# Optimization experiments

Measured on AMD Instinct MI355X. Metric: run time of the kernel, lower is better.

## Reference

```python
import jax, jax.numpy as jnp
import numpy as np

HEADS = 8
DIM_HEADS = 64
M_DIM = 512
X_DIM = 512
MEM_NUM = 512
N = 16384
PERCENT = 0.25
LAY_NUMBER = 2       # outer refinement iterations
CROSS_LAYERS = 2     # layers inside M_cross_layers
EPS = 1e-5


def setup_inputs() -> dict:
    key = jax.random.key(0)
    ks = jax.random.split(key, 8)
    data = jax.random.normal(ks[0], (N, X_DIM), dtype=jnp.float32)
    Memory = jax.random.normal(ks[1], (MEM_NUM, M_DIM), dtype=jnp.float32)
    # to_kv: Linear(X_dim, 2*kv_dim, bias=False); kv_dim = heads*dim_heads
    Wkv = jax.random.normal(ks[2], (X_DIM, 2 * HEADS * DIM_HEADS), dtype=jnp.float32) * 0.02
    # per cross layer: to_q (no bias) and mutl_heads (with bias)
    Wq = jax.random.normal(ks[3], (CROSS_LAYERS, M_DIM, HEADS * DIM_HEADS), dtype=jnp.float32) * 0.02
    Wm = jax.random.normal(ks[4], (CROSS_LAYERS, HEADS * DIM_HEADS, M_DIM), dtype=jnp.float32) * 0.02
    bm = jnp.zeros((CROSS_LAYERS, M_DIM), dtype=jnp.float32)
    return {"data": data, "Memory": Memory, "Wkv": Wkv, "Wq": Wq, "Wm": Wm, "bm": bm, "istest": 0}


def _layer_norm(x):
    # F.layer_norm over last dim, no affine params
    mu = jnp.mean(x, axis=-1, keepdims=True)
    var = jnp.var(x, axis=-1, keepdims=True)
    return (x - mu) * jax.lax.rsqrt(var + EPS)


def _cross_layer(M, X, Wkv, Wq_l, Wm_l, bm_l):
    # cross_att + residual + layernorm (SublayerConnection); FFN is dead code in source
    q = (M @ Wq_l).reshape(MEM_NUM, HEADS, DIM_HEADS).transpose(1, 0, 2)      # [h, m, dh]
    kv = X @ Wkv                                                              # [n, 2*h*dh]
    k, v = jnp.split(kv, 2, axis=-1)
    k = k.reshape(-1, HEADS, DIM_HEADS).transpose(1, 0, 2)                    # [h, n, dh]
    v = v.reshape(-1, HEADS, DIM_HEADS).transpose(1, 0, 2)
    sim = jnp.einsum('hid,hjd->hij', q, k) * (DIM_HEADS ** -0.5)              # [h, m, n]
    att = jax.nn.softmax(sim, axis=-1)
    o = jnp.einsum('hij,hjd->hid', att, v)                                    # [h, m, dh]
    o = o.transpose(1, 0, 2).reshape(MEM_NUM, HEADS * DIM_HEADS)
    out = o @ Wm_l + bm_l                                                     # [m, M_dim]
    return _layer_norm(out + M)


def _cross_layers(M, X, Wkv, Wq, Wm, bm):
    for l in range(CROSS_LAYERS):
        M = _cross_layer(M, X, Wkv, Wq[l], Wm[l], bm[l])
    return M


def _calucate_sim(data, M):
    # per-sample landmark similarity: max scaled dot product against memory rows
    logits = (data @ M.T) * (DIM_HEADS ** -0.5)   # [N, mem]
    return jnp.max(logits, axis=-1)               # [N]


def _calucate_emb(data, M):
    logits = (data @ M.T) * (DIM_HEADS ** -0.5)   # [N, mem]
    logp = jax.nn.log_softmax(logits, axis=-1)
    p = jnp.exp(logp)
    out_ebs = p @ M                               # soft memory readout [N, M_dim]
    result_loss = -jnp.mean(jnp.max(logp, axis=-1))
    lse = jax.scipy.special.logsumexp(logits, axis=-1)
    zloss = jnp.mean(lse ** 2)                    # router-style z-loss
    return out_ebs, result_loss, zloss


def _select(data, sim_M, k):
    _, top_idx = jax.lax.top_k(sim_M, k)
    X = jnp.zeros_like(data)
    return X.at[top_idx].set(data[top_idx])


def reference(data, Memory, Wkv, Wq, Wm, bm, istest):
    M = Memory
    sim_M = _calucate_sim(data, M)
    percent_count = int(data.shape[0] * PERCENT)
    if not istest:
        X = _select(data, sim_M, percent_count)
        for _ in range(LAY_NUMBER):
            M = _cross_layers(M, X, Wkv, Wq, Wm, bm)
            sim_M = _calucate_sim(data, M)
            X = _select(data, sim_M, percent_count)
    out_ebs, result_loss, zloss = _calucate_emb(data, M)
    return (sim_M, out_ebs, result_loss, zloss)
```

## Files before the change

### kernel.cpp

```cpp
#include <hip/hip_runtime.h>
#include <cstdint>

#define N_DATA 16384
#define DIM 512
#define MEM 512
#define KSEL 4096
#define NH 8
#define DH 64
#define KVDIM 1024
#define SCALE 0.125f
#define ZCNT 12288.0f
#define LN_EPS 1e-5f
#define NSPLIT 4

typedef unsigned short u16;
using short8 = __attribute__((ext_vector_type(8))) short;
using f32x4  = __attribute__((ext_vector_type(4))) float;

__device__ __forceinline__ unsigned fenc(float x) {
    unsigned u = __float_as_uint(x);
    return (u & 0x80000000u) ? ~u : (u | 0x80000000u);
}
__device__ __forceinline__ u16 f2bf(float x) {
    unsigned u = __float_as_uint(x);
    u += 0x7fffu + ((u >> 16) & 1u);
    return (u16)(u >> 16);
}
__device__ __forceinline__ float bf2f(u16 h) { return __uint_as_float(((unsigned)h) << 16); }

__device__ __forceinline__ float waveSum(float v) {
#pragma unroll
    for (int o = 32; o > 0; o >>= 1) v += __shfl_down(v, o, 64);
    return v;
}
__device__ float blockSum(float v) {
    __shared__ float sh[4];
    __syncthreads();
    v = waveSum(v);
    if ((threadIdx.x & 63) == 0) sh[threadIdx.x >> 6] = v;
    __syncthreads();
    if (threadIdx.x == 0) { float s = sh[0]; for (int i = 1; i < 4; ++i) s += sh[i]; sh[0] = s; }
    __syncthreads();
    return sh[0];
}

template<int ROWS, int NW, bool GATHER>
__device__ __forceinline__ void stage_tile(const u16* __restrict__ src, int ld, int k0,
                                           int row0, const int* __restrict__ gidx,
                                           u16* lds, int wave)
{
    constexpr int NI = ROWS / 16;
    const int lane = threadIdx.x & 63;
#pragma unroll
    for (int i = wave; i < NI; i += NW) {
        const int ch = i * 64 + lane;
        const int r = ch >> 2, cc = ch & 3;
        int rg = row0 + r;
        if (GATHER) rg = gidx[rg];
        const u16* g = src + (long)rg * ld + k0 + cc * 8;
        u16* l = lds + i * 512;
        __builtin_amdgcn_global_load_lds((const __attribute__((address_space(1))) void*)g,
                                         (__attribute__((address_space(3))) void*)l,
                                         16, 0, 0);
    }
}

template<int WM, int WN, bool GATHER, int EPI, bool BIAS>
__global__ __launch_bounds__(WM * WN * 64)
void mfma_gemm(const u16* __restrict__ A, const u16* __restrict__ B,
               const float* __restrict__ bias, const int* __restrict__ gidx,
               void* __restrict__ Cv, unsigned* __restrict__ simenc,
               int K, int lda, int ldb, int ldc,
               long zsA, long zsB, long zsC, int zdiv, long zsplitC, float alpha)
{
    constexpr int BM = WM * 64, BN = WN * 64, NW = WM * WN;
    __shared__ __align__(16) u16 As[BM * 32];
    __shared__ __align__(16) u16 Bs[BN * 32];

    const int t = threadIdx.x;
    const int wave = t >> 6, lane = t & 63;
    const int wr = wave / WN, wc = wave % WN;
    const int l15 = lane & 15, l4 = lane >> 4;
    const int bm0 = blockIdx.x * BM, bn0 = blockIdx.y * BN;
    const int zs = (int)blockIdx.z % zdiv;
    const int zh = (int)blockIdx.z / zdiv;
    A += (long)zh * zsA;
    B += (long)zh * zsB;

    f32x4 acc[4][4];
#pragma unroll
    for (int i = 0; i < 4; ++i)
#pragma unroll
        for (int j = 0; j < 4; ++j)
#pragma unroll
            for (int r = 0; r < 4; ++r) acc[i][j][r] = 0.f;

    const int Kd = K / zdiv;
    const int kbeg = zs * Kd;
    for (int k0 = kbeg; k0 < kbeg + Kd; k0 += 32) {
        stage_tile<BM, NW, GATHER>(A, lda, k0, bm0, gidx, As, wave);
        stage_tile<BN, NW, false>(B, ldb, k0, bn0, nullptr, Bs, wave);
        __syncthreads();
        short8 a[4], b[4];
#pragma unroll
        for (int fm = 0; fm < 4; ++fm)
            a[fm] = *(const short8*)(As + (wr * 64 + fm * 16 + l15) * 32 + l4 * 8);
#pragma unroll
        for (int fn = 0; fn < 4; ++fn)
            b[fn] = *(const short8*)(Bs + (wc * 64 + fn * 16 + l15) * 32 + l4 * 8);
#pragma unroll
        for (int fm = 0; fm < 4; ++fm)
#pragma unroll
            for (int fn = 0; fn < 4; ++fn)
                acc[fm][fn] = __builtin_amdgcn_mfma_f32_16x16x32_bf16(a[fm], b[fn], acc[fm][fn], 0, 0, 0);
        __syncthreads();
    }

    if (EPI == 2) {
#pragma unroll
        for (int fm = 0; fm < 4; ++fm)
#pragma unroll
            for (int r = 0; r < 4; ++r) {
                float mx = acc[fm][0][r];
#pragma unroll
                for (int fn = 1; fn < 4; ++fn) mx = fmaxf(mx, acc[fm][fn][r]);
#pragma unroll
                for (int o = 8; o >= 1; o >>= 1) mx = fmaxf(mx, __shfl_xor(mx, o, 64));
                if (l15 == 0) {
                    const int row = bm0 + wr * 64 + fm * 16 + l4 * 4 + r;
                    atomicMax(simenc + row, fenc(alpha * mx));
                }
            }
    } else if (EPI == 0) {
        float* C = (float*)Cv + (long)zh * zsC + (long)zs * zsplitC;
#pragma unroll
        for (int fm = 0; fm < 4; ++fm)
#pragma unroll
            for (int fn = 0; fn < 4; ++fn)
#pragma unroll
                for (int r = 0; r < 4; ++r) {
                    const int row = bm0 + wr * 64 + fm * 16 + l4 * 4 + r;
                    const int col = bn0 + wc * 64 + fn * 16 + l15;
                    float v = alpha * acc[fm][fn][r];
                    if (BIAS) v += bias[col];
                    C[(long)row * ldc + col] = v;
                }
    } else {
        u16* C = (u16*)Cv + (long)zh * zsC + (long)zs * zsplitC;
#pragma unroll
        for (int fm = 0; fm < 4; ++fm)
#pragma unroll
            for (int fn = 0; fn < 4; ++fn)
#pragma unroll
                for (int r = 0; r < 4; ++r) {
                    const int row = bm0 + wr * 64 + fm * 16 + l4 * 4 + r;
                    const int col = bn0 + wc * 64 + fn * 16 + l15;
                    float v = alpha * acc[fm][fn][r];
                    if (BIAS) v += bias[col];
                    C[(long)row * ldc + col] = f2bf(v);
                }
    }
}

__global__ __launch_bounds__(512)
void mfma_gemm_sm(const u16* __restrict__ A, const u16* __restrict__ B,
                  u16* __restrict__ Obf, float* __restrict__ simf,
                  float* __restrict__ lse, float* __restrict__ mlp, float alpha)
{
    __shared__ __align__(16) u16 As[64 * 32];
    __shared__ __align__(16) u16 Bs[512 * 32];
    const int t = threadIdx.x, wave = t >> 6, lane = t & 63;
    const int wc = wave;
    const int l15 = lane & 15, l4 = lane >> 4;
    const int bm0 = blockIdx.x * 64;

    f32x4 acc[4][4];
#pragma unroll
    for (int i = 0; i < 4; ++i)
#pragma unroll
        for (int j = 0; j < 4; ++j)
#pragma unroll
            for (int r = 0; r < 4; ++r) acc[i][j][r] = 0.f;

    for (int k0 = 0; k0 < 512; k0 += 32) {
        stage_tile<64, 8, false>(A, 512, k0, bm0, nullptr, As, wave);
        stage_tile<512, 8, false>(B, 512, k0, 0, nullptr, Bs, wave);
        __syncthreads();
        short8 a[4], b[4];
#pragma unroll
        for (int fm = 0; fm < 4; ++fm)
            a[fm] = *(const short8*)(As + (fm * 16 + l15) * 32 + l4 * 8);
#pragma unroll
        for (int fn = 0; fn < 4; ++fn)
            b[fn] = *(const short8*)(Bs + (wc * 64 + fn * 16 + l15) * 32 + l4 * 8);
#pragma unroll
        for (int fm = 0; fm < 4; ++fm)
#pragma unroll
            for (int fn = 0; fn < 4; ++fn)
                acc[fm][fn] = __builtin_amdgcn_mfma_f32_16x16x32_bf16(a[fm], b[fn], acc[fm][fn], 0, 0, 0);
        __syncthreads();
    }

    float* red  = (float*)As;
    float* rowv = (float*)Bs;

#pragma unroll
    for (int fm = 0; fm < 4; ++fm)
#pragma unroll
        for (int r = 0; r < 4; ++r) {
            float mx = alpha * acc[fm][0][r];
#pragma unroll
            for (int fn = 1; fn < 4; ++fn) mx = fmaxf(mx, alpha * acc[fm][fn][r]);
#pragma unroll
            for (int o = 1; o <= 8; o <<= 1) mx = fmaxf(mx, __shfl_xor(mx, o, 64));
            if (l15 == 0) red[(fm * 16 + l4 * 4 + r) * 8 + wc] = mx;
        }
    __syncthreads();
    if (t < 64) {
        float mx = red[t * 8];
#pragma unroll
        for (int j = 1; j < 8; ++j) mx = fmaxf(mx, red[t * 8 + j]);
        rowv[t] = mx;
    }
    __syncthreads();
#pragma unroll
    for (int fm = 0; fm < 4; ++fm)
#pragma unroll
        for (int r = 0; r < 4; ++r) {
            const int rl = fm * 16 + l4 * 4 + r;
            const float m = rowv[rl];
            float s = 0.f;
#pragma unroll
            for (int fn = 0; fn < 4; ++fn) s += __expf(alpha * acc[fm][fn][r] - m);
#pragma unroll
            for (int o = 1; o <= 8; o <<= 1) s += __shfl_xor(s, o, 64);
            if (l15 == 0) red[rl * 8 + wc] = s;
        }
    __syncthreads();
    if (t < 64) {
        float s = 0.f;
#pragma unroll
        for (int j = 0; j < 8; ++j) s += red[t * 8 + j];
        const float m = rowv[t];
        const float l = m + __logf(s);
        const int gr = bm0 + t;
        simf[gr] = m; lse[gr] = l; mlp[gr] = m - l;
        rowv[64 + t] = l;
    }
    __syncthreads();
#pragma unroll
    for (int fm = 0; fm < 4; ++fm)
#pragma unroll
        for (int r = 0; r < 4; ++r) {
            const int rl = fm * 16 + l4 * 4 + r;
            const float l = rowv[64 + rl];
#pragma unroll
            for (int fn = 0; fn < 4; ++fn) {
                const int col = wc * 64 + fn * 16 + l15;
                Obf[(long)(bm0 + rl) * 512 + col] = f2bf(__expf(alpha * acc[fm][fn][r] - l));
            }
        }
}

__global__ __launch_bounds__(256)
void flash_att(const u16* __restrict__ Mbf, const u16* __restrict__ WqT,
               const u16* __restrict__ KV, const u16* __restrict__ VT,
               float* __restrict__ oPart, float* __restrict__ mPart,
               float* __restrict__ lPart)
{
    __shared__ __align__(16) u16 Qs[64 * 64];
    __shared__ __align__(16) u16 Ks[2][64 * 64];
    __shared__ __align__(16) u16 Vs[2][64 * 64];
    __shared__ __align__(16) u16 Ps[4][16 * 72];

    const int qt = blockIdx.x, h = blockIdx.y, sp = blockIdx.z;
    const int t = threadIdx.x, wave = t >> 6, lane = t & 63;
    const int l15 = lane & 15, l4 = lane >> 4;

    const u16* Kg = KV + ((long)sp * 1024) * 1024 + h * 64;
    const u16* Vg = VT + ((long)h * 64) * 4096 + sp * 1024;

    auto stageKV = [&](int kt, int buf) {
        const u16* Kt = Kg + (long)(kt * 64) * 1024;
        const u16* Vt = Vg + kt * 64;
#pragma unroll
        for (int i = wave; i < 8; i += 4) {
            const int ch = i * 64 + lane, r = ch >> 3, s = ch & 7;
            __builtin_amdgcn_global_load_lds(
                (const __attribute__((address_space(1))) void*)(Kt + (long)r * 1024 + ((s ^ (r & 7)) * 8)),
                (__attribute__((address_space(3))) void*)(Ks[buf] + i * 512), 16, 0, 0);
        }
#pragma unroll
        for (int i = wave; i < 8; i += 4) {
            const int ch = i * 64 + lane, r = ch >> 3, s = ch & 7;
            __builtin_amdgcn_global_load_lds(
                (const __attribute__((address_space(1))) void*)(Vt + (long)r * 4096 + ((s ^ (r & 7)) * 8)),
                (__attribute__((address_space(3))) void*)(Vs[buf] + i * 512), 16, 0, 0);
        }
    };

    stageKV(0, 0);

    f32x4 accq[4];
#pragma unroll
    for (int fn = 0; fn < 4; ++fn)
#pragma unroll
        for (int r = 0; r < 4; ++r) accq[fn][r] = 0.f;
    {
        const u16* Ag = Mbf + (long)(qt * 64 + wave * 16 + l15) * 512 + l4 * 8;
        const u16* Bg = WqT + (long)(h * 64 + l15) * 512 + l4 * 8;
#pragma unroll 4
        for (int k0 = 0; k0 < 512; k0 += 32) {
            const short8 a = *(const short8*)(Ag + k0);
#pragma unroll
            for (int fn = 0; fn < 4; ++fn) {
                const short8 b = *(const short8*)(Bg + (long)fn * 16 * 512 + k0);
                accq[fn] = __builtin_amdgcn_mfma_f32_16x16x32_bf16(a, b, accq[fn], 0, 0, 0);
            }
        }
    }
#pragma unroll
    for (int fn = 0; fn < 4; ++fn)
#pragma unroll
        for (int r = 0; r < 4; ++r) {
            const int qrow = wave * 16 + l4 * 4 + r;
            const int col = fn * 16 + l15;
            Qs[qrow * 64 + (((col >> 3) ^ (qrow & 7)) << 3) + (col & 7)] = f2bf(accq[fn][r]);
        }
    __syncthreads();

    const int qr = wave * 16 + l15;
    short8 qf0 = *(const short8*)(Qs + qr * 64 + ((0 * 4 + l4) ^ (qr & 7)) * 8);
    short8 qf1 = *(const short8*)(Qs + qr * 64 + ((1 * 4 + l4) ^ (qr & 7)) * 8);

    float m = -3.0e38f, lsum = 0.f;
    f32x4 acc_o[4];
#pragma unroll
    for (int nf = 0; nf < 4; ++nf)
#pragma unroll
        for (int r = 0; r < 4; ++r) acc_o[nf][r] = 0.f;

    u16* myP = &Ps[wave][0];
    constexpr int NT = KSEL / 64 / NSPLIT;
    int cur = 0;

    for (int kt = 0; kt < NT; ++kt) {
        if (kt + 1 < NT) stageKV(kt + 1, cur ^ 1);
        const u16* Kc = Ks[cur];
        const u16* Vc = Vs[cur];
        f32x4 acc_s[4];
#pragma unroll
        for (int mf = 0; mf < 4; ++mf) {
#pragma unroll
            for (int r = 0; r < 4; ++r) acc_s[mf][r] = 0.f;
            const int kr = mf * 16 + l15;
            const short8 ka0 = *(const short8*)(Kc + kr * 64 + ((0 * 4 + l4) ^ (kr & 7)) * 8);
            const short8 ka1 = *(const short8*)(Kc + kr * 64 + ((1 * 4 + l4) ^ (kr & 7)) * 8);
            acc_s[mf] = __builtin_amdgcn_mfma_f32_16x16x32_bf16(ka0, qf0, acc_s[mf], 0, 0, 0);
            acc_s[mf] = __builtin_amdgcn_mfma_f32_16x16x32_bf16(ka1, qf1, acc_s[mf], 0, 0, 0);
        }
        float sv[16];
#pragma unroll
        for (int mf = 0; mf < 4; ++mf)
#pragma unroll
            for (int r = 0; r < 4; ++r) sv[mf * 4 + r] = SCALE * acc_s[mf][r];
        float pm = sv[0];
#pragma unroll
        for (int j = 1; j < 16; ++j) pm = fmaxf(pm, sv[j]);
        pm = fmaxf(pm, __shfl_xor(pm, 16, 64));
        pm = fmaxf(pm, __shfl_xor(pm, 32, 64));
        const float mnew = fmaxf(m, pm);
        const float corr = __expf(m - mnew);
        float rs = 0.f;
#pragma unroll
        for (int j = 0; j < 16; ++j) { sv[j] = __expf(sv[j] - mnew); rs += sv[j]; }
        rs += __shfl_xor(rs, 16, 64);
        rs += __shfl_xor(rs, 32, 64);
        lsum = lsum * corr + rs;
        m = mnew;
        const float cf0 = __shfl(corr, l4 * 4 + 0, 64);
        const float cf1 = __shfl(corr, l4 * 4 + 1, 64);
        const float cf2 = __shfl(corr, l4 * 4 + 2, 64);
        const float cf3 = __shfl(corr, l4 * 4 + 3, 64);
#pragma unroll
        for (int nf = 0; nf < 4; ++nf) {
            acc_o[nf][0] *= cf0; acc_o[nf][1] *= cf1;
            acc_o[nf][2] *= cf2; acc_o[nf][3] *= cf3;
        }
#pragma unroll
        for (int mf = 0; mf < 4; ++mf) {
            ushort4 pw;
            pw.x = f2bf(sv[mf * 4 + 0]); pw.y = f2bf(sv[mf * 4 + 1]);
            pw.z = f2bf(sv[mf * 4 + 2]); pw.w = f2bf(sv[mf * 4 + 3]);
            *(ushort4*)(myP + l15 * 72 + mf * 16 + l4 * 4) = pw;
        }
#pragma unroll
        for (int ks = 0; ks < 2; ++ks) {
            const short8 pa = *(const short8*)(myP + l15 * 72 + ks * 32 + l4 * 8);
#pragma unroll
            for (int nf = 0; nf < 4; ++nf) {
                const int dr = nf * 16 + l15;
                const short8 vb = *(const short8*)(Vc + dr * 64 + ((ks * 4 + l4) ^ (dr & 7)) * 8);
                acc_o[nf] = __builtin_amdgcn_mfma_f32_16x16x32_bf16(pa, vb, acc_o[nf], 0, 0, 0);
            }
        }
        __syncthreads();
        cur ^= 1;
    }

    float* ob = oPart + (((long)sp * NH + h) * 8 + qt) * 4096;
#pragma unroll
    for (int nf = 0; nf < 4; ++nf)
#pragma unroll
        for (int r = 0; r < 4; ++r)
            ob[(wave * 16 + l4 * 4 + r) * 64 + nf * 16 + l15] = acc_o[nf][r];
    if (lane < 16) {
        const int qi = wave * 16 + lane;
        mPart[((sp * NH + h) * 8 + qt) * 64 + qi] = m;
        lPart[((sp * NH + h) * 8 + qt) * 64 + qi] = lsum;
    }
}

__global__ __launch_bounds__(256)
void flash_combine(const float* __restrict__ oPart, const float* __restrict__ mPart,
                   const float* __restrict__ lPart, u16* __restrict__ o_bf)
{
    const int qt = blockIdx.x & 7, h = blockIdx.x >> 3;
    const int t = threadIdx.x;
    const int q = t >> 2, d0 = (t & 3) << 4;
    float mi[NSPLIT], li[NSPLIT];
#pragma unroll
    for (int sp = 0; sp < NSPLIT; ++sp) {
        const int sb = ((sp * NH + h) * 8 + qt) * 64 + q;
        mi[sp] = mPart[sb];
        li[sp] = lPart[sb];
    }
    float ms = 0.f;
#pragma unroll
    for (int sp = 0; sp < NSPLIT; ++sp) ms = fmaxf(ms, mi[sp]);
    float denom = ZCNT * __expf(-ms);
    float f[NSPLIT];
#pragma unroll
    for (int sp = 0; sp < NSPLIT; ++sp) { f[sp] = __expf(mi[sp] - ms); denom += li[sp] * f[sp]; }
    const float inv = 1.f / denom;
    float o[16];
#pragma unroll
    for (int j = 0; j < 16; ++j) o[j] = 0.f;
#pragma unroll
    for (int sp = 0; sp < NSPLIT; ++sp) {
        const float* ob = oPart + (((long)sp * NH + h) * 8 + qt) * 4096 + q * 64 + d0;
        const float fs = f[sp] * inv;
#pragma unroll
        for (int j = 0; j < 16; j += 4) {
            const float4 v = *(const float4*)(ob + j);
            o[j] += fs * v.x; o[j + 1] += fs * v.y; o[j + 2] += fs * v.z; o[j + 3] += fs * v.w;
        }
    }
    u16* op = o_bf + (qt * 64 + q) * 512 + h * 64 + d0;
#pragma unroll
    for (int j = 0; j < 16; j += 4) {
        ushort4 w4;
        w4.x = f2bf(o[j]); w4.y = f2bf(o[j + 1]); w4.z = f2bf(o[j + 2]); w4.w = f2bf(o[j + 3]);
        *(ushort4*)(op + j) = w4;
    }
}

__global__ __launch_bounds__(256)
void conv_f32_bf(const float* __restrict__ s, u16* __restrict__ d, int n)
{
    const int i = (blockIdx.x * 256 + threadIdx.x) * 4;
    if (i >= n) return;
    const float4 v = *(const float4*)(s + i);
    ushort4 o;
    o.x = f2bf(v.x); o.y = f2bf(v.y); o.z = f2bf(v.z); o.w = f2bf(v.w);
    *(ushort4*)(d + i) = o;
}

template<bool INBF>
__global__ __launch_bounds__(256)
void transpose_bf(const void* __restrict__ Sv, u16* __restrict__ D,
                  int Rr, int Cc, int ldS)
{
    __shared__ float tile[32][33];
    const int c0 = blockIdx.x * 32, r0 = blockIdx.y * 32;
    const int tx = threadIdx.x & 31, ty = threadIdx.x >> 5;
#pragma unroll
    for (int j = 0; j < 32; j += 8) {
        const int r = r0 + ty + j, c = c0 + tx;
        float v = INBF ? bf2f(((const u16*)Sv)[(long)r * ldS + c])
                       : ((const float*)Sv)[(long)r * ldS + c];
        tile[ty + j][tx] = v;
    }
    __syncthreads();
#pragma unroll
    for (int j = 0; j < 32; j += 8) {
        const int cO = c0 + ty + j, rO = r0 + tx;
        D[(long)cO * Rr + rO] = f2bf(tile[tx][ty + j]);
    }
}

__global__ __launch_bounds__(256)
void transpose_w4(const float* __restrict__ Wq, const float* __restrict__ Wm,
                  u16* __restrict__ WqT, u16* __restrict__ WmT)
{
    const int z = blockIdx.z;
    const float* S = (z < 2) ? (Wq + (long)z * DIM * DIM) : (Wm + (long)(z - 2) * DIM * DIM);
    u16* D = (z < 2) ? (WqT + (long)z * DIM * DIM) : (WmT + (long)(z - 2) * DIM * DIM);
    __shared__ float tile[32][33];
    const int c0 = blockIdx.x * 32, r0 = blockIdx.y * 32;
    const int tx = threadIdx.x & 31, ty = threadIdx.x >> 5;
#pragma unroll
    for (int j = 0; j < 32; j += 8)
        tile[ty + j][tx] = S[(long)(r0 + ty + j) * DIM + c0 + tx];
    __syncthreads();
#pragma unroll
    for (int j = 0; j < 32; j += 8)
        D[(long)(c0 + ty + j) * DIM + r0 + tx] = f2bf(tile[tx][ty + j]);
}

__device__ __forceinline__ unsigned scan1024_excl(unsigned v, unsigned* wsum)
{
    const int lane = threadIdx.x & 63, wv = threadIdx.x >> 6;
    __syncthreads();
    unsigned x = v;
#pragma unroll
    for (int o = 1; o < 64; o <<= 1) {
        unsigned y = __shfl_up(x, o, 64);
        if (lane >= o) x += y;
    }
    if (lane == 63) wsum[wv] = x;
    __syncthreads();
    if (threadIdx.x < 16) {
        unsigned w2 = wsum[threadIdx.x];
#pragma unroll
        for (int o = 1; o < 16; o <<= 1) {
            unsigned y = __shfl_up(w2, o, 64);
            if ((int)threadIdx.x >= o) w2 += y;
        }
        wsum[threadIdx.x] = w2;
    }
    __syncthreads();
    const unsigned off = (wv > 0) ? wsum[wv - 1] : 0u;
    return off + x - v;
}

#define SEL_T 1024
#define SEL_CH (N_DATA / SEL_T)
__global__ __launch_bounds__(SEL_T)
void select_topk(const unsigned* __restrict__ key, int* __restrict__ idxo, int k)
{
    __shared__ unsigned whist[16][256];
    __shared__ unsigned hist[256];
    __shared__ unsigned wsum[16];
    __shared__ unsigned sh_bin, sh_r;
    const int t = threadIdx.x;
    const int wv = t >> 6;
    const int base = t * SEL_CH;

    unsigned kreg[SEL_CH];
#pragma unroll
    for (int c = 0; c < SEL_CH; ++c) kreg[c] = key[base + c];

    unsigned prefix = 0, mask = 0;
    unsigned r = (unsigned)k;
    for (int p = 3; p >= 0; --p) {
        __syncthreads();
        for (int i = t; i < 16 * 256; i += SEL_T) ((unsigned*)whist)[i] = 0u;
        __syncthreads();
#pragma unroll
        for (int c = 0; c < SEL_CH; ++c) {
            const unsigned kv = kreg[c];
            if ((kv & mask) == prefix)
                atomicAdd(&whist[wv][(kv >> (p * 8)) & 255u], 1u);
        }
        __syncthreads();
        if (t < 256) {
            unsigned s = 0;
#pragma unroll
            for (int wq = 0; wq < 16; ++wq) s += whist[wq][t];
            hist[t] = s;
        }
        __syncthreads();
        if (t < 64) {
            const int b0 = 255 - 4 * t;
            const unsigned c = hist[b0] + hist[b0 - 1] + hist[b0 - 2] + hist[b0 - 3];
            unsigned x = c;
#pragma unroll
            for (int o = 1; o < 64; o <<= 1) {
                unsigned y = __shfl_up(x, o, 64);
                if (t >= o) x += y;
            }
            const unsigned pre = x - c;
            if (pre < r && r <= x) {
                unsigned cum = pre;
#pragma unroll
                for (int j = 0; j < 4; ++j) {
                    const int b = b0 - j;
                    cum += hist[b];
                    if (cum >= r) { sh_bin = (unsigned)b; sh_r = r - (cum - hist[b]); break; }
                }
            }
        }
        __syncthreads();
        prefix |= sh_bin << (p * 8);
        mask |= 255u << (p * 8);
        r = sh_r;
    }
    const unsigned thr = prefix;
    const unsigned ties = r;

    unsigned ceq = 0;
#pragma unroll
    for (int c = 0; c < SEL_CH; ++c) ceq += (kreg[c] == thr) ? 1u : 0u;
    const unsigned eqbase = scan1024_excl(ceq, wsum);
    unsigned eq = eqbase, csel = 0;
#pragma unroll
    for (int c = 0; c < SEL_CH; ++c) {
        const unsigned kv = kreg[c];
        bool s;
        if (kv == thr) { s = (eq < ties); ++eq; }
        else s = (kv > thr);
        csel += s ? 1u : 0u;
    }
    unsigned pos = scan1024_excl(csel, wsum);
    eq = eqbase;
#pragma unroll
    for (int c = 0; c < SEL_CH; ++c) {
        const unsigned kv = kreg[c];
        bool s;
        if (kv == thr) { s = (eq < ties); ++eq; }
        else s = (kv > thr);
        if (s) idxo[pos++] = base + c;
    }
}

__global__ __launch_bounds__(256)
void ln_add_k(const float* __restrict__ outp, const float* __restrict__ Min,
              float* __restrict__ Mout, u16* __restrict__ Mbf)
{
    const int r = blockIdx.x;
    const int t = threadIdx.x;
    float x0 = outp[r * DIM + t] + Min[r * DIM + t];
    float x1 = outp[r * DIM + t + 256] + Min[r * DIM + t + 256];
    float s = blockSum(x0 + x1);
    float s2 = blockSum(x0 * x0 + x1 * x1);
    const float mu = s * (1.f / DIM);
    const float var = s2 * (1.f / DIM) - mu * mu;
    const float rs = rsqrtf(var + LN_EPS);
    const float y0 = (x0 - mu) * rs, y1 = (x1 - mu) * rs;
    Mout[r * DIM + t] = y0;
    Mout[r * DIM + t + 256] = y1;
    Mbf[r * DIM + t] = f2bf(y0);
    Mbf[r * DIM + t + 256] = f2bf(y1);
}

__global__ __launch_bounds__(256)
void reduce_loss(const float* __restrict__ lse, const float* __restrict__ mlp,
                 float* __restrict__ o2)
{
    const int t = threadIdx.x;
    float s1 = 0.f, s2 = 0.f;
    for (int i = t; i < N_DATA; i += 256) { s1 += mlp[i]; float l = lse[i]; s2 += l * l; }
    s1 = blockSum(s1);
    s2 = blockSum(s2);
    if (t == 0) { o2[0] = -s1 * (1.f / N_DATA); o2[1] = s2 * (1.f / N_DATA); }
}

extern "C" void kernel_launch(void* const* d_in, const int* in_sizes, int n_in,
                              void* d_out, int out_size, void* d_ws, size_t ws_size,
                              hipStream_t stream)
{
    (void)in_sizes; (void)n_in; (void)out_size; (void)ws_size;
    const float* data   = (const float*)d_in[0];
    const float* Memory = (const float*)d_in[1];
    const float* Wkv    = (const float*)d_in[2];
    const float* Wq     = (const float*)d_in[3];
    const float* Wm     = (const float*)d_in[4];
    const float* bm     = (const float*)d_in[5];
    float* out = (float*)d_out;

    char* w = (char*)d_ws;
    unsigned* simenc = (unsigned*)(w + 0);
    int*   idx     = (int*)  (w + 65536);
    float* lse     = (float*)(w + 81920);
    float* mlp     = (float*)(w + 147456);
    float* Ma      = (float*)(w + 262144);
    float* Mb      = (float*)(w + 1310720);
    u16*   Mbf0    = (u16*)  (w + 2359296);
    u16*   MT_bf   = (u16*)  (w + 2883584);
    u16*   WqT_bf  = (u16*)  (w + 3407872);
    u16*   WmT_bf  = (u16*)  (w + 4456448);
    u16*   WkvT_bf = (u16*)  (w + 5505024);
    u16*   o_bf    = (u16*)  (w + 7077888);
    float* outp    = (float*)(w + 7602176);
    u16*   data_bf = (u16*)  (w + 8650752);
    u16*   kvsel_bf= (u16*)  (w + 25427968);
    u16*   vT_bf   = (u16*)  (w + 33816576);
    float* oPart   = (float*)(w + 38010880);
    float* mPart   = (float*)(w + 42205184);
    float* lPart   = (float*)(w + 42270720);
    u16*   logits_bf = (u16*)(w + 54788096);
    u16*   Mbfa    = (u16*)  (w + 88342528);
    u16*   Mbfb    = (u16*)  (w + 88866816);

    conv_f32_bf<<<(N_DATA * DIM / 4 + 255) / 256, 256, 0, stream>>>(data, data_bf, N_DATA * DIM);
    conv_f32_bf<<<(DIM * DIM / 4 + 255) / 256, 256, 0, stream>>>(Memory, Mbf0, DIM * DIM);
    transpose_bf<false><<<dim3(KVDIM / 32, DIM / 32), 256, 0, stream>>>(Wkv, WkvT_bf, DIM, KVDIM, KVDIM);
    transpose_w4<<<dim3(16, 16, 4), 256, 0, stream>>>(Wq, Wm, WqT_bf, WmT_bf);

    auto sim_select_kv = [&](const u16* Mrows_bf) {
        hipMemsetAsync(simenc, 0, N_DATA * 4, stream);
        mfma_gemm<2, 2, false, 2, false><<<dim3(128, 4, 1), 256, 0, stream>>>(
            data_bf, Mrows_bf, nullptr, nullptr, nullptr, simenc,
            DIM, DIM, DIM, 0, 0, 0, 0, 1, 0, SCALE);
        select_topk<<<1, SEL_T, 0, stream>>>(simenc, idx, KSEL);
        mfma_gemm<2, 2, true, 1, false><<<dim3(32, 8, 1), 256, 0, stream>>>(
            data_bf, WkvT_bf, nullptr, idx, kvsel_bf, nullptr,
            DIM, DIM, DIM, KVDIM, 0, 0, 0, 1, 0, 1.0f);
        transpose_bf<true><<<dim3(DIM / 32, KSEL / 32), 256, 0, stream>>>(
            kvsel_bf + DIM, vT_bf, KSEL, DIM, KVDIM);
    };

    auto cross = [&](const float* Mcur, const u16* Mcur_bf, float* Mnext, u16* Mnext_bf, int l) {
        flash_att<<<dim3(8, NH, NSPLIT), 256, 0, stream>>>(
            Mcur_bf, WqT_bf + (long)l * DIM * DIM, kvsel_bf, vT_bf, oPart, mPart, lPart);
        flash_combine<<<64, 256, 0, stream>>>(oPart, mPart, lPart, o_bf);
        mfma_gemm<2, 2, false, 0, true><<<dim3(4, 4, 1), 256, 0, stream>>>(
            o_bf, WmT_bf + (long)l * DIM * DIM, bm + (long)l * DIM, nullptr, outp, nullptr,
            DIM, DIM, DIM, DIM, 0, 0, 0, 1, 0, 1.0f);
        ln_add_k<<<DIM, 256, 0, stream>>>(outp, Mcur, Mnext, Mnext_bf);
    };

    const float* Mcur = Memory;
    const u16*  curbf = Mbf0;
    float* Mnext = Ma;
    u16*   nextbf = Mbfa;
    sim_select_kv(curbf);
    for (int it = 0; it < 2; ++it) {
        for (int l = 0; l < 2; ++l) {
            cross(Mcur, curbf, Mnext, nextbf, l);
            Mcur = Mnext; curbf = nextbf;
            Mnext = (Mcur == Ma) ? Mb : Ma;
            nextbf = (curbf == Mbfa) ? Mbfb : Mbfa;
        }
        if (it == 0) sim_select_kv(curbf);
    }

    mfma_gemm_sm<<<N_DATA / 64, 512, 0, stream>>>(
        data_bf, curbf, logits_bf, out, lse, mlp, SCALE);
    transpose_bf<false><<<dim3(16, 16), 256, 0, stream>>>(Mcur, MT_bf, MEM, DIM, DIM);
    mfma_gemm<2, 2, false, 0, false><<<dim3(128, 4, 1), 256, 0, stream>>>(
        logits_bf, MT_bf, nullptr, nullptr, out + N_DATA, nullptr,
        MEM, MEM, MEM, DIM, 0, 0, 0, 1, 0, 1.0f);
    reduce_loss<<<1, 256, 0, stream>>>(lse, mlp, out + N_DATA + (long)N_DATA * DIM);
}
```

Before: 389.7 us.

## Fuse softmax readout GEMM into logits kernel and combine into Wm GEMM

The final logits/softmax kernel now keeps the bf16 probability tile in shared memory and runs the P@M readout GEMM in the same block, so the 16384x512 probability matrix is no longer written to and re-read from global memory. Separately, the flash-attention split combine is folded into the Wm projection GEMM's A-tile staging, which removes the flash_combine launch and the o_bf round trip. In exchange, the fused kernel uses about 66KB more LDS, which may limit occupancy, and the Wm GEMM now recomputes the split combine while staging its A tiles.

```diff
diff --git a/kernel.cpp b/kernel.cpp
--- a/kernel.cpp
+++ b/kernel.cpp
@@ -163,12 +163,14 @@
 }
 
 __global__ __launch_bounds__(512)
-void mfma_gemm_sm(const u16* __restrict__ A, const u16* __restrict__ B,
-                  u16* __restrict__ Obf, float* __restrict__ simf,
-                  float* __restrict__ lse, float* __restrict__ mlp, float alpha)
+void gemm_sm_pm(const u16* __restrict__ A, const u16* __restrict__ B,
+                const u16* __restrict__ BT, float* __restrict__ outEb,
+                float* __restrict__ simf, float* __restrict__ lse,
+                float* __restrict__ mlp, float alpha)
 {
     __shared__ __align__(16) u16 As[64 * 32];
     __shared__ __align__(16) u16 Bs[512 * 32];
+    __shared__ __align__(16) u16 Pl[64 * 520];
     const int t = threadIdx.x, wave = t >> 6, lane = t & 63;
     const int wc = wave;
     const int l15 = lane & 15, l4 = lane >> 4;
@@ -257,9 +259,144 @@
 #pragma unroll
             for (int fn = 0; fn < 4; ++fn) {
                 const int col = wc * 64 + fn * 16 + l15;
-                Obf[(long)(bm0 + rl) * 512 + col] = f2bf(__expf(alpha * acc[fm][fn][r] - l));
+                Pl[rl * 520 + col] = f2bf(__expf(alpha * acc[fm][fn][r] - l));
             }
         }
+    __syncthreads();
+
+    f32x4 acc2[4][4];
+#pragma unroll
+    for (int i = 0; i < 4; ++i)
+#pragma unroll
+        for (int j = 0; j < 4; ++j)
+#pragma unroll
+            for (int r = 0; r < 4; ++r) acc2[i][j][r] = 0.f;
+
+    for (int k0 = 0; k0 < 512; k0 += 32) {
+        stage_tile<512, 8, false>(BT, 512, k0, 0, nullptr, Bs, wave);
+        __syncthreads();
+        short8 a[4], b[4];
+#pragma unroll
+        for (int fm = 0; fm < 4; ++fm)
+            a[fm] = *(const short8*)(Pl + (fm * 16 + l15) * 520 + k0 + l4 * 8);
+#pragma unroll
+        for (int fn = 0; fn < 4; ++fn)
+            b[fn] = *(const short8*)(Bs + (wc * 64 + fn * 16 + l15) * 32 + l4 * 8);
+#pragma unroll
+        for (int fm = 0; fm < 4; ++fm)
+#pragma unroll
+            for (int fn = 0; fn < 4; ++fn)
+                acc2[fm][fn] = __builtin_amdgcn_mfma_f32_16x16x32_bf16(a[fm], b[fn], acc2[fm][fn], 0, 0, 0);
+        __syncthreads();
+    }
+#pragma unroll
+    for (int fm = 0; fm < 4; ++fm)
+#pragma unroll
+        for (int fn = 0; fn < 4; ++fn)
+#pragma unroll
+            for (int r = 0; r < 4; ++r) {
+                const int row = bm0 + fm * 16 + l4 * 4 + r;
+                const int col = wc * 64 + fn * 16 + l15;
+                outEb[(long)row * 512 + col] = acc2[fm][fn][r];
+            }
+}
+
+__global__ __launch_bounds__(256)
+void wm_combine_gemm(const float* __restrict__ oPart, const float* __restrict__ mPart,
+                     const float* __restrict__ lPart, const u16* __restrict__ BT,
+                     const float* __restrict__ bias, float* __restrict__ Cout)
+{
+    __shared__ __align__(16) u16 As[128 * 32];
+    __shared__ __align__(16) u16 Bs[128 * 32];
+    __shared__ float wTab[NSPLIT][128][8];
+    const int t = threadIdx.x, wave = t >> 6, lane = t & 63;
+    const int wr = wave >> 1, wc = wave & 1;
+    const int l15 = lane & 15, l4 = lane >> 4;
+    const int bm0 = blockIdx.x * 128, bn0 = blockIdx.y * 128;
+
+    for (int i = t; i < 128 * 8; i += 256) {
+        const int row = i >> 3, h = i & 7;
+        const int m = bm0 + row, qt = m >> 6, q = m & 63;
+        float mi[NSPLIT], li[NSPLIT];
+#pragma unroll
+        for (int sp = 0; sp < NSPLIT; ++sp) {
+            const int sb = ((sp * NH + h) * 8 + qt) * 64 + q;
+            mi[sp] = mPart[sb];
+            li[sp] = lPart[sb];
+        }
+        float ms = 0.f;
+#pragma unroll
+        for (int sp = 0; sp < NSPLIT; ++sp) ms = fmaxf(ms, mi[sp]);
+        float denom = ZCNT * __expf(-ms);
+        float f[NSPLIT];
+#pragma unroll
+        for (int sp = 0; sp < NSPLIT; ++sp) { f[sp] = __expf(mi[sp] - ms); denom += li[sp] * f[sp]; }
+        const float inv = 1.f / denom;
+#pragma unroll
+        for (int sp = 0; sp < NSPLIT; ++sp) wTab[sp][row][h] = f[sp] * inv;
+    }
+    __syncthreads();
+
+    f32x4 acc[4][4];
+#pragma unroll
+    for (int i = 0; i < 4; ++i)
+#pragma unroll
+        for (int j = 0; j < 4; ++j)
+#pragma unroll
+            for (int r = 0; r < 4; ++r) acc[i][j][r] = 0.f;
+
+    for (int k0 = 0; k0 < 512; k0 += 32) {
+        const int h = k0 >> 6, d0 = k0 & 63;
+#pragma unroll
+        for (int cchunk = 0; cchunk < 2; ++cchunk) {
+            const int c = cchunk * 256 + t;
+            const int row = c >> 2, seg = c & 3;
+            const int m = bm0 + row, qt = m >> 6, q = m & 63;
+            const int d = d0 + seg * 8;
+            float o8[8];
+#pragma unroll
+            for (int j = 0; j < 8; ++j) o8[j] = 0.f;
+#pragma unroll
+            for (int sp = 0; sp < NSPLIT; ++sp) {
+                const float wgt = wTab[sp][row][h];
+                const float* ob = oPart + (((long)sp * NH + h) * 8 + qt) * 4096 + q * 64 + d;
+                const float4 v0 = *(const float4*)(ob);
+                const float4 v1 = *(const float4*)(ob + 4);
+                o8[0] += wgt * v0.x; o8[1] += wgt * v0.y; o8[2] += wgt * v0.z; o8[3] += wgt * v0.w;
+                o8[4] += wgt * v1.x; o8[5] += wgt * v1.y; o8[6] += wgt * v1.z; o8[7] += wgt * v1.w;
+            }
+            short8 pw;
+#pragma unroll
+            for (int j = 0; j < 8; ++j) pw[j] = (short)f2bf(o8[j]);
+            *(short8*)(As + row * 32 + seg * 8) = pw;
+        }
+        stage_tile<128, 4, false>(BT, 512, k0, bn0, nullptr, Bs, wave);
+        __syncthreads();
+        short8 a[4], b[4];
+#pragma unroll
+        for (int fm = 0; fm < 4; ++fm)
+            a[fm] = *(const short8*)(As + (wr * 64 + fm * 16 + l15) * 32 + l4 * 8);
+#pragma unroll
+        for (int fn = 0; fn < 4; ++fn)
+            b[fn] = *(const short8*)(Bs + (wc * 64 + fn * 16 + l15) * 32 + l4 * 8);
+#pragma unroll
+        for (int fm = 0; fm < 4; ++fm)
+#pragma unroll
+            for (int fn = 0; fn < 4; ++fn)
+                acc[fm][fn] = __builtin_amdgcn_mfma_f32_16x16x32_bf16(a[fm], b[fn], acc[fm][fn], 0, 0, 0);
+        __syncthreads();
+    }
+
+#pragma unroll
+    for (int fm = 0; fm < 4; ++fm)
+#pragma unroll
+        for (int fn = 0; fn < 4; ++fn)
+#pragma unroll
+            for (int r = 0; r < 4; ++r) {
+                const int row = bm0 + wr * 64 + fm * 16 + l4 * 4 + r;
+                const int col = bn0 + wc * 64 + fn * 16 + l15;
+                Cout[(long)row * 512 + col] = acc[fm][fn][r] + bias[col];
+            }
 }
 
 __global__ __launch_bounds__(256)
@@ -418,50 +555,6 @@
         const int qi = wave * 16 + lane;
         mPart[((sp * NH + h) * 8 + qt) * 64 + qi] = m;
         lPart[((sp * NH + h) * 8 + qt) * 64 + qi] = lsum;
-    }
-}
-
-__global__ __launch_bounds__(256)
-void flash_combine(const float* __restrict__ oPart, const float* __restrict__ mPart,
-                   const float* __restrict__ lPart, u16* __restrict__ o_bf)
-{
-    const int qt = blockIdx.x & 7, h = blockIdx.x >> 3;
-    const int t = threadIdx.x;
-    const int q = t >> 2, d0 = (t & 3) << 4;
-    float mi[NSPLIT], li[NSPLIT];
-#pragma unroll
-    for (int sp = 0; sp < NSPLIT; ++sp) {
-        const int sb = ((sp * NH + h) * 8 + qt) * 64 + q;
-        mi[sp] = mPart[sb];
-        li[sp] = lPart[sb];
-    }
-    float ms = 0.f;
-#pragma unroll
-    for (int sp = 0; sp < NSPLIT; ++sp) ms = fmaxf(ms, mi[sp]);
-    float denom = ZCNT * __expf(-ms);
-    float f[NSPLIT];
-#pragma unroll
-    for (int sp = 0; sp < NSPLIT; ++sp) { f[sp] = __expf(mi[sp] - ms); denom += li[sp] * f[sp]; }
-    const float inv = 1.f / denom;
-    float o[16];
-#pragma unroll
-    for (int j = 0; j < 16; ++j) o[j] = 0.f;
-#pragma unroll
-    for (int sp = 0; sp < NSPLIT; ++sp) {
-        const float* ob = oPart + (((long)sp * NH + h) * 8 + qt) * 4096 + q * 64 + d0;
-        const float fs = f[sp] * inv;
-#pragma unroll
-        for (int j = 0; j < 16; j += 4) {
-            const float4 v = *(const float4*)(ob + j);
-            o[j] += fs * v.x; o[j + 1] += fs * v.y; o[j + 2] += fs * v.z; o[j + 3] += fs * v.w;
-        }
-    }
-    u16* op = o_bf + (qt * 64 + q) * 512 + h * 64 + d0;
-#pragma unroll
-    for (int j = 0; j < 16; j += 4) {
-        ushort4 w4;
-        w4.x = f2bf(o[j]); w4.y = f2bf(o[j + 1]); w4.z = f2bf(o[j + 2]); w4.w = f2bf(o[j + 3]);
-        *(ushort4*)(op + j) = w4;
     }
 }
 
@@ -691,7 +784,6 @@
     u16*   WqT_bf  = (u16*)  (w + 3407872);
     u16*   WmT_bf  = (u16*)  (w + 4456448);
     u16*   WkvT_bf = (u16*)  (w + 5505024);
-    u16*   o_bf    = (u16*)  (w + 7077888);
     float* outp    = (float*)(w + 7602176);
     u16*   data_bf = (u16*)  (w + 8650752);
     u16*   kvsel_bf= (u16*)  (w + 25427968);
@@ -699,7 +791,6 @@
     float* oPart   = (float*)(w + 38010880);
     float* mPart   = (float*)(w + 42205184);
     float* lPart   = (float*)(w + 42270720);
-    u16*   logits_bf = (u16*)(w + 54788096);
     u16*   Mbfa    = (u16*)  (w + 88342528);
     u16*   Mbfb    = (u16*)  (w + 88866816);
 
@@ -724,10 +815,8 @@
     auto cross = [&](const float* Mcur, const u16* Mcur_bf, float* Mnext, u16* Mnext_bf, int l) {
         flash_att<<<dim3(8, NH, NSPLIT), 256, 0, stream>>>(
             Mcur_bf, WqT_bf + (long)l * DIM * DIM, kvsel_bf, vT_bf, oPart, mPart, lPart);
-        flash_combine<<<64, 256, 0, stream>>>(oPart, mPart, lPart, o_bf);
-        mfma_gemm<2, 2, false, 0, true><<<dim3(4, 4, 1), 256, 0, stream>>>(
-            o_bf, WmT_bf + (long)l * DIM * DIM, bm + (long)l * DIM, nullptr, outp, nullptr,
-            DIM, DIM, DIM, DIM, 0, 0, 0, 1, 0, 1.0f);
+        wm_combine_gemm<<<dim3(4, 4), 256, 0, stream>>>(
+            oPart, mPart, lPart, WmT_bf + (long)l * DIM * DIM, bm + (long)l * DIM, outp);
         ln_add_k<<<DIM, 256, 0, stream>>>(outp, Mcur, Mnext, Mnext_bf);
     };
 
@@ -746,11 +835,8 @@
         if (it == 0) sim_select_kv(curbf);
     }
 
-    mfma_gemm_sm<<<N_DATA / 64, 512, 0, stream>>>(
-        data_bf, curbf, logits_bf, out, lse, mlp, SCALE);
     transpose_bf<false><<<dim3(16, 16), 256, 0, stream>>>(Mcur, MT_bf, MEM, DIM, DIM);
-    mfma_gemm<2, 2, false, 0, false><<<dim3(128, 4, 1), 256, 0, stream>>>(
-        logits_bf, MT_bf, nullptr, nullptr, out + N_DATA, nullptr,
-        MEM, MEM, MEM, DIM, 0, 0, 0, 1, 0, 1.0f);
+    gemm_sm_pm<<<N_DATA / 64, 512, 0, stream>>>(
+        data_bf, curbf, MT_bf, out + N_DATA, out, lse, mlp, SCALE);
     reduce_loss<<<1, 256, 0, stream>>>(lse, mlp, out + N_DATA + (long)N_DATA * DIM);
 }
```

After: 440.6 us. 1.13x slower.

## Fuse prologue conversions, V transpose into KV GEMM, and Wm GEMM with layernorm

Applied to the files above, without the earlier changes.

Merges the four prologue conversion/transpose launches into a single kernel. The gathered KV projection GEMM now writes the V half directly in transposed layout, which removes the separate bf16 transpose kernel. The Wm projection GEMM is fused with the bias, residual add and layernorm into one kernel, so the fp32 intermediate round-trip and a launch per cross layer go away. The fused wmln kernel uses only 32 blocks, each staging the full 512-column B tile per K step, which may limit parallelism.

```diff
diff --git a/kernel.cpp b/kernel.cpp
--- a/kernel.cpp
+++ b/kernel.cpp
@@ -70,6 +70,7 @@
 void mfma_gemm(const u16* __restrict__ A, const u16* __restrict__ B,
                const float* __restrict__ bias, const int* __restrict__ gidx,
                void* __restrict__ Cv, unsigned* __restrict__ simenc,
+               u16* __restrict__ vTo,
                int K, int lda, int ldb, int ldc,
                long zsA, long zsB, long zsC, int zdiv, long zsplitC, float alpha)
 {
@@ -145,7 +146,7 @@
                     if (BIAS) v += bias[col];
                     C[(long)row * ldc + col] = v;
                 }
-    } else {
+    } else if (EPI == 1) {
         u16* C = (u16*)Cv + (long)zh * zsC + (long)zs * zsplitC;
 #pragma unroll
         for (int fm = 0; fm < 4; ++fm)
@@ -159,6 +160,34 @@
                     if (BIAS) v += bias[col];
                     C[(long)row * ldc + col] = f2bf(v);
                 }
+    } else {
+        if (bn0 < 512) {
+            u16* C = (u16*)Cv;
+#pragma unroll
+            for (int fm = 0; fm < 4; ++fm)
+#pragma unroll
+                for (int fn = 0; fn < 4; ++fn)
+#pragma unroll
+                    for (int r = 0; r < 4; ++r) {
+                        const int row = bm0 + wr * 64 + fm * 16 + l4 * 4 + r;
+                        const int col = bn0 + wc * 64 + fn * 16 + l15;
+                        C[(long)row * ldc + col] = f2bf(alpha * acc[fm][fn][r]);
+                    }
+        } else {
+#pragma unroll
+            for (int fm = 0; fm < 4; ++fm)
+#pragma unroll
+                for (int fn = 0; fn < 4; ++fn) {
+                    const int d = bn0 + wc * 64 + fn * 16 + l15 - 512;
+                    const int row0 = bm0 + wr * 64 + fm * 16 + l4 * 4;
+                    ushort4 pw;
+                    pw.x = f2bf(alpha * acc[fm][fn][0]);
+                    pw.y = f2bf(alpha * acc[fm][fn][1]);
+                    pw.z = f2bf(alpha * acc[fm][fn][2]);
+                    pw.w = f2bf(alpha * acc[fm][fn][3]);
+                    *(ushort4*)(vTo + (long)d * 4096 + row0) = pw;
+                }
+        }
     }
 }
 
@@ -260,6 +289,82 @@
                 Obf[(long)(bm0 + rl) * 512 + col] = f2bf(__expf(alpha * acc[fm][fn][r] - l));
             }
         }
+}
+
+__global__ __launch_bounds__(512)
+void wmln(const u16* __restrict__ A, const u16* __restrict__ BT,
+          const float* __restrict__ bias, const float* __restrict__ Min,
+          float* __restrict__ Mout, u16* __restrict__ Mbf)
+{
+    __shared__ __align__(16) u16 As[16 * 32];
+    __shared__ __align__(16) u16 Bs[512 * 32];
+    __shared__ float red[16][8], red2[16][8], rowv[32];
+    const int t = threadIdx.x, wave = t >> 6, lane = t & 63;
+    const int wc = wave;
+    const int l15 = lane & 15, l4 = lane >> 4;
+    const int bm0 = blockIdx.x * 16;
+
+    f32x4 acc[4];
+#pragma unroll
+    for (int fn = 0; fn < 4; ++fn)
+#pragma unroll
+        for (int r = 0; r < 4; ++r) acc[fn][r] = 0.f;
+
+    for (int k0 = 0; k0 < 512; k0 += 32) {
+        stage_tile<16, 8, false>(A, 512, k0, bm0, nullptr, As, wave);
+        stage_tile<512, 8, false>(BT, 512, k0, 0, nullptr, Bs, wave);
+        __syncthreads();
+        const short8 a = *(const short8*)(As + l15 * 32 + l4 * 8);
+#pragma unroll
+        for (int fn = 0; fn < 4; ++fn) {
+            const short8 b = *(const short8*)(Bs + (wc * 64 + fn * 16 + l15) * 32 + l4 * 8);
+            acc[fn] = __builtin_amdgcn_mfma_f32_16x16x32_bf16(a, b, acc[fn], 0, 0, 0);
+        }
+        __syncthreads();
+    }
+
+    float v[4][4];
+#pragma unroll
+    for (int fn = 0; fn < 4; ++fn) {
+        const int col = wc * 64 + fn * 16 + l15;
+        const float bi = bias[col];
+#pragma unroll
+        for (int r = 0; r < 4; ++r) {
+            const int row = bm0 + l4 * 4 + r;
+            v[fn][r] = acc[fn][r] + bi + Min[(long)row * 512 + col];
+        }
+    }
+#pragma unroll
+    for (int r = 0; r < 4; ++r) {
+        float s = 0.f, s2 = 0.f;
+#pragma unroll
+        for (int fn = 0; fn < 4; ++fn) { const float x = v[fn][r]; s += x; s2 += x * x; }
+#pragma unroll
+        for (int o = 1; o <= 8; o <<= 1) { s += __shfl_xor(s, o, 64); s2 += __shfl_xor(s2, o, 64); }
+        if (l15 == 0) { red[l4 * 4 + r][wc] = s; red2[l4 * 4 + r][wc] = s2; }
+    }
+    __syncthreads();
+    if (t < 16) {
+        float s = 0.f, s2 = 0.f;
+#pragma unroll
+        for (int j = 0; j < 8; ++j) { s += red[t][j]; s2 += red2[t][j]; }
+        const float mu = s * (1.f / 512.f);
+        const float var = s2 * (1.f / 512.f) - mu * mu;
+        rowv[t] = mu;
+        rowv[16 + t] = rsqrtf(var + LN_EPS);
+    }
+    __syncthreads();
+#pragma unroll
+    for (int fn = 0; fn < 4; ++fn) {
+        const int col = wc * 64 + fn * 16 + l15;
+#pragma unroll
+        for (int r = 0; r < 4; ++r) {
+            const int rl = l4 * 4 + r;
+            const float y = (v[fn][r] - rowv[rl]) * rowv[16 + rl];
+            Mout[(long)(bm0 + rl) * 512 + col] = y;
+            Mbf [(long)(bm0 + rl) * 512 + col] = f2bf(y);
+        }
+    }
 }
 
 __global__ __launch_bounds__(256)
@@ -465,57 +570,78 @@
     }
 }
 
+#define PRO_DATA 8192
+#define PRO_W4   1024
+#define PRO_WKV  512
+#define PRO_MEM  256
 __global__ __launch_bounds__(256)
-void conv_f32_bf(const float* __restrict__ s, u16* __restrict__ d, int n)
-{
-    const int i = (blockIdx.x * 256 + threadIdx.x) * 4;
-    if (i >= n) return;
-    const float4 v = *(const float4*)(s + i);
-    ushort4 o;
-    o.x = f2bf(v.x); o.y = f2bf(v.y); o.z = f2bf(v.z); o.w = f2bf(v.w);
-    *(ushort4*)(d + i) = o;
-}
-
-template<bool INBF>
+void prologue(const float* __restrict__ data, const float* __restrict__ Memory,
+              const float* __restrict__ Wkv, const float* __restrict__ Wq,
+              const float* __restrict__ Wm,
+              u16* __restrict__ data_bf, u16* __restrict__ Mbf,
+              u16* __restrict__ WkvT, u16* __restrict__ WqT, u16* __restrict__ WmT)
+{
+    __shared__ float tile[32][33];
+    const int bid = blockIdx.x, t = threadIdx.x;
+    if (bid < PRO_DATA) {
+        const int i = (bid * 256 + t) * 4;
+        const float4 v = *(const float4*)(data + i);
+        ushort4 o;
+        o.x = f2bf(v.x); o.y = f2bf(v.y); o.z = f2bf(v.z); o.w = f2bf(v.w);
+        *(ushort4*)(data_bf + i) = o;
+        return;
+    }
+    int b2 = bid - PRO_DATA;
+    const int tx = t & 31, ty = t >> 5;
+    if (b2 < PRO_W4) {
+        const int z = b2 >> 8, q = b2 & 255;
+        const float* S = (z < 2) ? (Wq + (long)z * DIM * DIM) : (Wm + (long)(z - 2) * DIM * DIM);
+        u16* D = (z < 2) ? (WqT + (long)z * DIM * DIM) : (WmT + (long)(z - 2) * DIM * DIM);
+        const int c0 = (q & 15) * 32, r0 = (q >> 4) * 32;
+#pragma unroll
+        for (int j = 0; j < 32; j += 8)
+            tile[ty + j][tx] = S[(long)(r0 + ty + j) * DIM + c0 + tx];
+        __syncthreads();
+#pragma unroll
+        for (int j = 0; j < 32; j += 8)
+            D[(long)(c0 + ty + j) * DIM + r0 + tx] = f2bf(tile[tx][ty + j]);
+        return;
+    }
+    b2 -= PRO_W4;
+    if (b2 < PRO_WKV) {
+        const int c0 = (b2 & 31) * 32, r0 = (b2 >> 5) * 32;
+#pragma unroll
+        for (int j = 0; j < 32; j += 8)
+            tile[ty + j][tx] = Wkv[(long)(r0 + ty + j) * KVDIM + c0 + tx];
+        __syncthreads();
+#pragma unroll
+        for (int j = 0; j < 32; j += 8)
+            WkvT[(long)(c0 + ty + j) * DIM + r0 + tx] = f2bf(tile[tx][ty + j]);
+        return;
+    }
+    b2 -= PRO_WKV;
+    {
+        const int i = (b2 * 256 + t) * 4;
+        const float4 v = *(const float4*)(Memory + i);
+        ushort4 o;
+        o.x = f2bf(v.x); o.y = f2bf(v.y); o.z = f2bf(v.z); o.w = f2bf(v.w);
+        *(ushort4*)(Mbf + i) = o;
+    }
+}
+
 __global__ __launch_bounds__(256)
-void transpose_bf(const void* __restrict__ Sv, u16* __restrict__ D,
-                  int Rr, int Cc, int ldS)
+void transpose_f32bf(const float* __restrict__ S, u16* __restrict__ D, int Rr, int ldS)
 {
     __shared__ float tile[32][33];
     const int c0 = blockIdx.x * 32, r0 = blockIdx.y * 32;
     const int tx = threadIdx.x & 31, ty = threadIdx.x >> 5;
 #pragma unroll
-    for (int j = 0; j < 32; j += 8) {
-        const int r = r0 + ty + j, c = c0 + tx;
-        float v = INBF ? bf2f(((const u16*)Sv)[(long)r * ldS + c])
-                       : ((const float*)Sv)[(long)r * ldS + c];
-        tile[ty + j][tx] = v;
-    }
-    __syncthreads();
-#pragma unroll
-    for (int j = 0; j < 32; j += 8) {
-        const int cO = c0 + ty + j, rO = r0 + tx;
-        D[(long)cO * Rr + rO] = f2bf(tile[tx][ty + j]);
-    }
-}
-
-__global__ __launch_bounds__(256)
-void transpose_w4(const float* __restrict__ Wq, const float* __restrict__ Wm,
-                  u16* __restrict__ WqT, u16* __restrict__ WmT)
-{
-    const int z = blockIdx.z;
-    const float* S = (z < 2) ? (Wq + (long)z * DIM * DIM) : (Wm + (long)(z - 2) * DIM * DIM);
-    u16* D = (z < 2) ? (WqT + (long)z * DIM * DIM) : (WmT + (long)(z - 2) * DIM * DIM);
-    __shared__ float tile[32][33];
-    const int c0 = blockIdx.x * 32, r0 = blockIdx.y * 32;
-    const int tx = threadIdx.x & 31, ty = threadIdx.x >> 5;
-#pragma unroll
     for (int j = 0; j < 32; j += 8)
-        tile[ty + j][tx] = S[(long)(r0 + ty + j) * DIM + c0 + tx];
+        tile[ty + j][tx] = S[(long)(r0 + ty + j) * ldS + c0 + tx];
     __syncthreads();
 #pragma unroll
     for (int j = 0; j < 32; j += 8)
-        D[(long)(c0 + ty + j) * DIM + r0 + tx] = f2bf(tile[tx][ty + j]);
+        D[(long)(c0 + ty + j) * Rr + r0 + tx] = f2bf(tile[tx][ty + j]);
 }
 
 __device__ __forceinline__ unsigned scan1024_excl(unsigned v, unsigned* wsum)
@@ -632,26 +758,6 @@
         else s = (kv > thr);
         if (s) idxo[pos++] = base + c;
     }
-}
-
-__global__ __launch_bounds__(256)
-void ln_add_k(const float* __restrict__ outp, const float* __restrict__ Min,
-              float* __restrict__ Mout, u16* __restrict__ Mbf)
-{
-    const int r = blockIdx.x;
-    const int t = threadIdx.x;
-    float x0 = outp[r * DIM + t] + Min[r * DIM + t];
-    float x1 = outp[r * DIM + t + 256] + Min[r * DIM + t + 256];
-    float s = blockSum(x0 + x1);
-    float s2 = blockSum(x0 * x0 + x1 * x1);
-    const float mu = s * (1.f / DIM);
-    const float var = s2 * (1.f / DIM) - mu * mu;
-    const float rs = rsqrtf(var + LN_EPS);
-    const float y0 = (x0 - mu) * rs, y1 = (x1 - mu) * rs;
-    Mout[r * DIM + t] = y0;
-    Mout[r * DIM + t + 256] = y1;
-    Mbf[r * DIM + t] = f2bf(y0);
-    Mbf[r * DIM + t + 256] = f2bf(y1);
 }
 
 __global__ __launch_bounds__(256)
@@ -692,7 +798,6 @@
     u16*   WmT_bf  = (u16*)  (w + 4456448);
     u16*   WkvT_bf = (u16*)  (w + 5505024);
     u16*   o_bf    = (u16*)  (w + 7077888);
-    float* outp    = (float*)(w + 7602176);
     u16*   data_bf = (u16*)  (w + 8650752);
     u16*   kvsel_bf= (u16*)  (w + 25427968);
     u16*   vT_bf   = (u16*)  (w + 33816576);
@@ -703,32 +808,26 @@
     u16*   Mbfa    = (u16*)  (w + 88342528);
     u16*   Mbfb    = (u16*)  (w + 88866816);
 
-    conv_f32_bf<<<(N_DATA * DIM / 4 + 255) / 256, 256, 0, stream>>>(data, data_bf, N_DATA * DIM);
-    conv_f32_bf<<<(DIM * DIM / 4 + 255) / 256, 256, 0, stream>>>(Memory, Mbf0, DIM * DIM);
-    transpose_bf<false><<<dim3(KVDIM / 32, DIM / 32), 256, 0, stream>>>(Wkv, WkvT_bf, DIM, KVDIM, KVDIM);
-    transpose_w4<<<dim3(16, 16, 4), 256, 0, stream>>>(Wq, Wm, WqT_bf, WmT_bf);
+    prologue<<<PRO_DATA + PRO_W4 + PRO_WKV + PRO_MEM, 256, 0, stream>>>(
+        data, Memory, Wkv, Wq, Wm, data_bf, Mbf0, WkvT_bf, WqT_bf, WmT_bf);
 
     auto sim_select_kv = [&](const u16* Mrows_bf) {
         hipMemsetAsync(simenc, 0, N_DATA * 4, stream);
         mfma_gemm<2, 2, false, 2, false><<<dim3(128, 4, 1), 256, 0, stream>>>(
-            data_bf, Mrows_bf, nullptr, nullptr, nullptr, simenc,
+            data_bf, Mrows_bf, nullptr, nullptr, nullptr, simenc, nullptr,
             DIM, DIM, DIM, 0, 0, 0, 0, 1, 0, SCALE);
         select_topk<<<1, SEL_T, 0, stream>>>(simenc, idx, KSEL);
-        mfma_gemm<2, 2, true, 1, false><<<dim3(32, 8, 1), 256, 0, stream>>>(
-            data_bf, WkvT_bf, nullptr, idx, kvsel_bf, nullptr,
+        mfma_gemm<2, 2, true, 3, false><<<dim3(32, 8, 1), 256, 0, stream>>>(
+            data_bf, WkvT_bf, nullptr, idx, kvsel_bf, nullptr, vT_bf,
             DIM, DIM, DIM, KVDIM, 0, 0, 0, 1, 0, 1.0f);
-        transpose_bf<true><<<dim3(DIM / 32, KSEL / 32), 256, 0, stream>>>(
-            kvsel_bf + DIM, vT_bf, KSEL, DIM, KVDIM);
     };
 
     auto cross = [&](const float* Mcur, const u16* Mcur_bf, float* Mnext, u16* Mnext_bf, int l) {
         flash_att<<<dim3(8, NH, NSPLIT), 256, 0, stream>>>(
             Mcur_bf, WqT_bf + (long)l * DIM * DIM, kvsel_bf, vT_bf, oPart, mPart, lPart);
         flash_combine<<<64, 256, 0, stream>>>(oPart, mPart, lPart, o_bf);
-        mfma_gemm<2, 2, false, 0, true><<<dim3(4, 4, 1), 256, 0, stream>>>(
-            o_bf, WmT_bf + (long)l * DIM * DIM, bm + (long)l * DIM, nullptr, outp, nullptr,
-            DIM, DIM, DIM, DIM, 0, 0, 0, 1, 0, 1.0f);
-        ln_add_k<<<DIM, 256, 0, stream>>>(outp, Mcur, Mnext, Mnext_bf);
+        wmln<<<32, 512, 0, stream>>>(
+            o_bf, WmT_bf + (long)l * DIM * DIM, bm + (long)l * DIM, Mcur, Mnext, Mnext_bf);
     };
 
     const float* Mcur = Memory;
@@ -748,9 +847,9 @@
 
     mfma_gemm_sm<<<N_DATA / 64, 512, 0, stream>>>(
         data_bf, curbf, logits_bf, out, lse, mlp, SCALE);
-    transpose_bf<false><<<dim3(16, 16), 256, 0, stream>>>(Mcur, MT_bf, MEM, DIM, DIM);
+    transpose_f32bf<<<dim3(16, 16), 256, 0, stream>>>(Mcur, MT_bf, MEM, DIM);
     mfma_gemm<2, 2, false, 0, false><<<dim3(128, 4, 1), 256, 0, stream>>>(
-        logits_bf, MT_bf, nullptr, nullptr, out + N_DATA, nullptr,
+        logits_bf, MT_bf, nullptr, nullptr, out + N_DATA, nullptr, nullptr,
         MEM, MEM, MEM, DIM, 0, 0, 0, 1, 0, 1.0f);
     reduce_loss<<<1, 256, 0, stream>>>(lse, mlp, out + N_DATA + (long)N_DATA * DIM);
 }
```

After: 381.6 us. 2.1% less time.
